# Performance work log

Hardware: AMD Instinct MI355X
Metric: run time of the kernel (lower is better)

The kernel has to match this reference:

```python
import jax, jax.numpy as jnp
import numpy as np

B = 32
N = 1024  # half_size == num_delays == num_wavelength
DELTA_TAU = 1.5e-15
W_CENTER = 1.175e15  # center_frequency / 2
PULSE_THRESHOLD = 0.01
PENALTY = 10.0
REAL_W = 1.0; IMAG_W = 1.0; INT_W = 1.0; PHASE_W = 1.0; FROG_W = 1.0
MSE_WSUM = REAL_W + IMAG_W + INT_W + PHASE_W

# Hilbert mask exactly as in the torch source (even N branch): H[N//2+1:]=2, H[N//2]=1
_Hm = np.zeros(N, dtype=np.float32)
_Hm[N // 2 + 1:] = 2.0
_Hm[N // 2] = 1.0
HILBERT_MASK = jnp.asarray(_Hm)

# precomputed circular-shift gather indices: shifted[m, j] = x[(j - delay[m]) mod N]
_delays = np.arange(-(N // 2), N // 2)
SHIFT_IDX = jnp.asarray((np.arange(N)[None, :] - _delays[:, None]) % N)  # [N, N] int
SHIFT_FACTOR = jnp.exp(-1j * jnp.asarray(2.0 * W_CENTER * DELTA_TAU * _delays, dtype=jnp.float32)).astype(jnp.complex64)  # [N]


def hilbert(x):  # x: [N] real -> [N] complex analytical signal
    xf = jnp.fft.fft(x)
    return jnp.fft.ifft(xf * HILBERT_MASK)


def shg_mat(a):  # a: [N] complex -> [N, N] complex SHG matrix (vectorized createSHGmat)
    shifted = a[SHIFT_IDX]                                  # [N, N] all circular shifts
    rows = a[None, :] * shifted * SHIFT_FACTOR[None, :]     # elementwise complex multiply
    f = jnp.fft.fft(jnp.fft.fftshift(rows, axes=-1), axis=-1)  # one batched FFT
    return DELTA_TAU * jnp.fft.fftshift(f, axes=-1)


def _first_last(mask):  # mask: [B, N] bool -> per-sample first/last significant index with fallback
    any_m = jnp.any(mask, axis=1)
    first = jnp.where(any_m, jnp.argmax(mask, axis=1), 0)
    last = jnp.where(any_m, N - 1 - jnp.argmax(mask[:, ::-1], axis=1), N - 1)
    return first, last


def setup_inputs() -> dict:
    key = jax.random.key(0)
    k1, k2, k3 = jax.random.split(key, 3)
    prediction = jax.random.normal(k1, (B, N), dtype=jnp.float32)
    label = jax.random.normal(k2, (B, 2 * N), dtype=jnp.float32)
    shg_matrix = jax.random.uniform(k3, (B, 1, N, N), dtype=jnp.float32)
    return {"prediction": prediction, "label": label, "shg_matrix": shg_matrix}


def reference(prediction, label, shg_matrix):
    pa = jax.vmap(hilbert)(prediction)          # [B, N] complex64
    pr, pi = pa.real, pa.imag
    lr, li = label[:, :N], label[:, N:]
    l_int = lr ** 2 + li ** 2
    p_int = pr ** 2 + pi ** 2
    l_ph = jnp.arctan2(li, lr)
    p_ph = jnp.arctan2(pi, pr)

    # ---- FROG error ----
    shg_pred = jnp.abs(jax.vmap(shg_mat)(pa)) ** 2              # [B, N, N]
    shg_pred = shg_pred / jnp.max(shg_pred, axis=(1, 2), keepdims=True)  # normalizeSHGmatrix
    t_ref = shg_matrix[:, 0]                                    # [B, N, N]
    sum1 = jnp.sum(shg_pred * t_ref, axis=(1, 2))
    sum2 = jnp.sum(t_ref * t_ref, axis=(1, 2))
    mu = sum1 / sum2
    r = jnp.sum(shg_pred - mu[:, None, None] * t_ref, axis=(1, 2)) ** 2
    norm = (N * N) * jnp.max(shg_pred, axis=(1, 2)) ** 2
    frog = jnp.where(r == 0.0, 0.0, jnp.sqrt(r / norm))         # [B]

    # ---- weighted masked MSE ----
    fr, lr_idx = _first_last(jnp.abs(lr) > PULSE_THRESHOLD)
    fi, li_idx = _first_last(jnp.abs(li) > PULSE_THRESHOLD)
    first = jnp.minimum(fr, fi)
    last = jnp.maximum(lr_idx, li_idx)
    ar = jnp.arange(N)[None, :]
    in_range = (ar >= first[:, None]) & (ar < last[:, None])    # [first:last] slice semantics
    phase_mask = in_range.astype(jnp.float32)
    pulse_mask = jnp.where(in_range, PENALTY, 1.0)

    mse_real = jnp.mean((pr - lr) ** 2 * pulse_mask, axis=1) * REAL_W
    mse_imag = jnp.mean((pi - li) ** 2 * pulse_mask, axis=1) * IMAG_W
    mse_int = jnp.mean((p_int - l_int) ** 2 * pulse_mask, axis=1) * INT_W
    mse_ph = jnp.mean((p_ph - l_ph) ** 2 * phase_mask, axis=1) * PHASE_W
    mse = (mse_real + mse_imag + mse_int + mse_ph) / MSE_WSUM

    return jnp.mean(mse + FROG_W * frog)
```

## Files before the change

### kernel.cpp

```cpp
#include <hip/hip_runtime.h>
#include <math.h>

#define N 1024
#define BATCH 32
#define NT 256
#define PADC(i) ((i) + ((i) >> 5))

#define WSYNC() asm volatile("s_waitcnt lgkmcnt(0)" ::: "memory")

typedef float2 cf;
__device__ __forceinline__ cf cadd(cf a, cf b){ return make_float2(a.x+b.x, a.y+b.y); }
__device__ __forceinline__ cf csub(cf a, cf b){ return make_float2(a.x-b.x, a.y-b.y); }
__device__ __forceinline__ cf cmul(cf a, cf b){ return make_float2(a.x*b.x - a.y*b.y, a.x*b.y + a.y*b.x); }

__device__ __forceinline__ cf twiddle(float jn){
    float s = __builtin_amdgcn_sinf(jn);
    float c = __builtin_amdgcn_cosf(jn);
    return make_float2(c, -s);
}

__device__ __forceinline__ int rev8(int q){
    int r = (int)(__brev((unsigned)q) >> 24);
    return ((r & 0x55) << 1) | ((r >> 1) & 0x55);
}
__device__ __forceinline__ int rev10(int m){
    int r = (int)(__brev((unsigned)m) >> 22);
    return ((r & 0x155) << 1) | ((r >> 1) & 0x155);
}

__device__ __forceinline__ void dif4(cf* w, int base, int q, float jn){
    cf x0 = w[PADC(base)];
    cf x1 = w[PADC(base + q)];
    cf x2 = w[PADC(base + 2*q)];
    cf x3 = w[PADC(base + 3*q)];
    cf A = cadd(x0,x2), Bs = cadd(x1,x3);
    cf C = csub(x0,x2), D = csub(x1,x3);
    cf Dmi = make_float2(D.y, -D.x);
    cf w1 = twiddle(jn);
    cf w2 = cmul(w1,w1);
    cf w3 = cmul(w2,w1);
    w[PADC(base)]       = cadd(A,Bs);
    w[PADC(base + q)]   = cmul(cadd(C,Dmi), w1);
    w[PADC(base + 2*q)] = cmul(csub(A,Bs), w2);
    w[PADC(base + 3*q)] = cmul(csub(C,Dmi), w3);
}

template<int LOG2N>
__device__ __forceinline__ void dif_stage(cf* w, int t){
    const int n = 1 << LOG2N, q = n >> 2;
    int j = t & (q - 1);
    int base = ((t >> (LOG2N - 2)) << LOG2N) + j;
    dif4(w, base, q, (float)j * (1.0f / (float)n));
}
template<int LOG2N>
__device__ __forceinline__ void dit_stage(cf* w, int t){
    const int n = 1 << LOG2N, q = n >> 2;
    int j = t & (q - 1);
    int base = ((t >> (LOG2N - 2)) << LOG2N) + j;
    cf x0 = w[PADC(base)];
    cf x1 = w[PADC(base + q)];
    cf x2 = w[PADC(base + 2*q)];
    cf x3 = w[PADC(base + 3*q)];
    cf w1 = twiddle((float)j * (1.0f / (float)n));
    cf w2 = cmul(w1,w1);
    cf w3 = cmul(w2,w1);
    x1 = cmul(x1,w1); x2 = cmul(x2,w2); x3 = cmul(x3,w3);
    cf A = cadd(x0,x2), Bs = cadd(x1,x3);
    cf C = csub(x0,x2), D = csub(x1,x3);
    cf Dmi = make_float2(D.y, -D.x);
    w[PADC(base)]       = cadd(A,Bs);
    w[PADC(base + q)]   = cadd(C,Dmi);
    w[PADC(base + 2*q)] = csub(A,Bs);
    w[PADC(base + 3*q)] = csub(C,Dmi);
}

__global__ __launch_bounds__(NT) void hilbert_k(const float* __restrict__ pred,
                                                const float* __restrict__ label,
                                                cf* __restrict__ a,
                                                cf* __restrict__ ca,
                                                float* __restrict__ mseJ) {
    __shared__ cf wk[1056];
    __shared__ float rbuf[4][4];
    __shared__ int ibuf[4][4];
    __shared__ int s_first, s_last;
    int t = threadIdx.x, b = blockIdx.x;
    for (int i = t; i < N; i += NT) wk[PADC(i)] = make_float2(pred[b * N + i], 0.f);
    __syncthreads();
    dif_stage<10>(wk, t); __syncthreads();
    dif_stage<8>(wk, t);  __syncthreads();
    dif_stage<6>(wk, t);  __syncthreads();
    dif_stage<4>(wk, t);  __syncthreads();
    dif_stage<2>(wk, t);  __syncthreads();
    for (int i = t; i < N; i += NT) {
        int k = rev10(i);
        float f = (k < 512) ? 0.f : ((k == 512) ? 1.f : 2.f);
        cf v = wk[PADC(i)];
        wk[PADC(i)] = make_float2(f * v.x, -f * v.y);
    }
    __syncthreads();
    dit_stage<2>(wk, t);  __syncthreads();
    dit_stage<4>(wk, t);  __syncthreads();
    dit_stage<6>(wk, t);  __syncthreads();
    dit_stage<8>(wk, t);  __syncthreads();
    dit_stage<10>(wk, t); __syncthreads();
    const float sc = 1.f / (float)N;
    for (int i = t; i < N; i += NT) {
        cf v = wk[PADC(i)];
        cf av = make_float2(v.x * sc, -v.y * sc);
        wk[PADC(i)] = av;
        a[b * N + i] = av;
        float p = (float)(3.525 * (double)(i - 512));
        float s_, c_;
        sincosf(p, &s_, &c_);
        ca[b * N + i] = make_float2(av.x * c_ + av.y * s_, av.y * c_ - av.x * s_);
    }
    __syncthreads();

    int w = t >> 6, lane = t & 63;
    int mnR = N, mxR = -1, mnI = N, mxI = -1;
    for (int n = t; n < N; n += NT) {
        float lr = label[b * 2 * N + n];
        float li = label[b * 2 * N + N + n];
        if (fabsf(lr) > 0.01f) { mnR = min(mnR, n); mxR = max(mxR, n); }
        if (fabsf(li) > 0.01f) { mnI = min(mnI, n); mxI = max(mxI, n); }
    }
    for (int o = 32; o > 0; o >>= 1) {
        mnR = min(mnR, __shfl_down(mnR, o));
        mxR = max(mxR, __shfl_down(mxR, o));
        mnI = min(mnI, __shfl_down(mnI, o));
        mxI = max(mxI, __shfl_down(mxI, o));
    }
    if (lane == 0) { ibuf[w][0] = mnR; ibuf[w][1] = mxR; ibuf[w][2] = mnI; ibuf[w][3] = mxI; }
    __syncthreads();
    if (t == 0) {
        int a0 = N, a1 = -1, a2 = N, a3 = -1;
        for (int i = 0; i < 4; ++i) {
            a0 = min(a0, ibuf[i][0]); a1 = max(a1, ibuf[i][1]);
            a2 = min(a2, ibuf[i][2]); a3 = max(a3, ibuf[i][3]);
        }
        int fr   = (a0 == N) ? 0 : a0;
        int lstR = (a1 < 0) ? (N - 1) : a1;
        int fi   = (a2 == N) ? 0 : a2;
        int lstI = (a3 < 0) ? (N - 1) : a3;
        s_first = min(fr, fi);
        s_last  = max(lstR, lstI);
    }
    __syncthreads();
    int first = s_first, last = s_last;

    float m_r = 0.f, m_i = 0.f, m_n = 0.f, m_p = 0.f;
    for (int n = t; n < N; n += NT) {
        cf p = wk[PADC(n)];
        float lr = label[b * 2 * N + n];
        float li = label[b * 2 * N + N + n];
        bool in = (n >= first) && (n < last);
        float pm  = in ? 10.f : 1.f;
        float phm = in ? 1.f : 0.f;
        float dr = p.x - lr, di = p.y - li;
        float dn = (p.x * p.x + p.y * p.y) - (lr * lr + li * li);
        float dp = atan2f(p.y, p.x) - atan2f(li, lr);
        m_r += dr * dr * pm;
        m_i += di * di * pm;
        m_n += dn * dn * pm;
        m_p += dp * dp * phm;
    }
    for (int o = 32; o > 0; o >>= 1) {
        m_r += __shfl_down(m_r, o);
        m_i += __shfl_down(m_i, o);
        m_n += __shfl_down(m_n, o);
        m_p += __shfl_down(m_p, o);
    }
    if (lane == 0) { rbuf[w][0] = m_r; rbuf[w][1] = m_i; rbuf[w][2] = m_n; rbuf[w][3] = m_p; }
    __syncthreads();
    if (t == 0) {
        float s = 0.f;
        for (int i = 0; i < 4; ++i) s += rbuf[i][0] + rbuf[i][1] + rbuf[i][2] + rbuf[i][3];
        mseJ[b] = s * (1.f / (float)N) * 0.25f;
    }
}

__global__ __launch_bounds__(NT) void shg_k(const cf* __restrict__ a,
                                            const cf* __restrict__ cag,
                                            const float* __restrict__ tref,
                                            float* __restrict__ Praw,
                                            float* __restrict__ Prt,
                                            float* __restrict__ Pmax,
                                            float* __restrict__ Pt,
                                            float* __restrict__ Ptt) {
    __shared__ cf wk[1056];
    __shared__ float rbuf[4][8];
    int t = threadIdx.x, bd = blockIdx.x;
    int b = bd >> 10, d = bd & 1023;

    {
        const cf* arow  = a   + b * N;
        const cf* carow = cag + b * N;
        cf x[4];
#pragma unroll
        for (int k = 0; k < 4; ++k) {
            int n1 = (t + 256 * k + 512) & 1023;
            int n2 = (t + 256 * k - d) & 1023;
            x[k] = cmul(carow[n1], arow[n2]);
        }
        cf A = cadd(x[0],x[2]), Bs = cadd(x[1],x[3]);
        cf C = csub(x[0],x[2]), D = csub(x[1],x[3]);
        cf Dmi = make_float2(D.y, -D.x);
        cf w1 = twiddle((float)t * (1.0f / 1024.0f));
        cf w2 = cmul(w1,w1);
        cf w3 = cmul(w2,w1);
        wk[PADC(t)]       = cadd(A,Bs);
        wk[PADC(t + 256)] = cmul(cadd(C,Dmi), w1);
        wk[PADC(t + 512)] = cmul(csub(A,Bs), w2);
        wk[PADC(t + 768)] = cmul(csub(C,Dmi), w3);
    }
    __syncthreads();
    dif4(wk, ((t >> 6) << 8) + (t & 63), 64, (float)(t & 63) * (1.0f / 256.0f)); WSYNC();
    dif4(wk, ((t >> 4) << 6) + (t & 15), 16, (float)(t & 15) * (1.0f / 64.0f));  WSYNC();
    dif4(wk, ((t >> 2) << 4) + (t & 3),   4, (float)(t & 3)  * (1.0f / 16.0f));  WSYNC();

    float sraw = 0.f, srt = 0.f, mx = 0.f, st = 0.f, stt = 0.f;
    const float* trow = tref + ((size_t)bd << 10);
    {
        int base = 4 * t;
        cf x0 = wk[PADC(base)], x1 = wk[PADC(base+1)];
        cf x2 = wk[PADC(base+2)], x3 = wk[PADC(base+3)];
        cf A = cadd(x0,x2), Bs = cadd(x1,x3);
        cf C = csub(x0,x2), D = csub(x1,x3);
        cf Dmi = make_float2(D.y, -D.x);
        cf y[4];
        y[0] = cadd(A,Bs); y[1] = cadd(C,Dmi); y[2] = csub(A,Bs); y[3] = csub(C,Dmi);
        int rq = rev8(t);
#pragma unroll
        for (int m = 0; m < 4; ++m) {
            float m2 = y[m].x * y[m].x + y[m].y * y[m].y;
            float tv = trow[(((m + 2) & 3) << 8) + rq];
            sraw += m2;
            srt += m2 * tv;
            mx = fmaxf(mx, m2);
            st += tv;
            stt += tv * tv;
        }
    }
    for (int o = 32; o > 0; o >>= 1) {
        sraw += __shfl_down(sraw, o);
        srt  += __shfl_down(srt, o);
        mx    = fmaxf(mx, __shfl_down(mx, o));
        st   += __shfl_down(st, o);
        stt  += __shfl_down(stt, o);
    }
    int w = t >> 6, lane = t & 63;
    if (lane == 0) {
        rbuf[w][0] = sraw; rbuf[w][1] = srt; rbuf[w][2] = mx;
        rbuf[w][3] = st;   rbuf[w][4] = stt;
    }
    __syncthreads();
    if (t == 0) {
        float a0 = 0.f, a1 = 0.f, a2 = 0.f, a3 = 0.f, a4 = 0.f;
        for (int i = 0; i < 4; ++i) {
            a0 += rbuf[i][0]; a1 += rbuf[i][1]; a2 = fmaxf(a2, rbuf[i][2]);
            a3 += rbuf[i][3]; a4 += rbuf[i][4];
        }
        Praw[bd] = a0; Prt[bd] = a1; Pmax[bd] = a2; Pt[bd] = a3; Ptt[bd] = a4;
    }
}

__global__ __launch_bounds__(NT) void loss_k(const float* __restrict__ Praw,
                                             const float* __restrict__ Prt,
                                             const float* __restrict__ Pmax,
                                             const float* __restrict__ Pt,
                                             const float* __restrict__ Ptt,
                                             const float* __restrict__ mseJ,
                                             float* __restrict__ out) {
    __shared__ float rbuf[4][8];
    int tid = threadIdx.x, b = blockIdx.x;
    int w = tid >> 6, lane = tid & 63;
    float sr = 0.f, srt = 0.f, mx = 0.f, st = 0.f, stt = 0.f;
    for (int i = tid; i < N; i += NT) {
        int idx = b * N + i;
        sr += Praw[idx]; srt += Prt[idx]; mx = fmaxf(mx, Pmax[idx]);
        st += Pt[idx];   stt += Ptt[idx];
    }
    for (int o = 32; o > 0; o >>= 1) {
        sr  += __shfl_down(sr, o);
        srt += __shfl_down(srt, o);
        mx   = fmaxf(mx, __shfl_down(mx, o));
        st  += __shfl_down(st, o);
        stt += __shfl_down(stt, o);
    }
    if (lane == 0) {
        rbuf[w][0] = sr; rbuf[w][1] = srt; rbuf[w][2] = mx;
        rbuf[w][3] = st; rbuf[w][4] = stt;
    }
    __syncthreads();
    if (tid == 0) {
        float A0 = 0.f, A1 = 0.f, A2 = 0.f, A3 = 0.f, A4 = 0.f;
        for (int i = 0; i < 4; ++i) {
            A0 += rbuf[i][0]; A1 += rbuf[i][1]; A2 = fmaxf(A2, rbuf[i][2]);
            A3 += rbuf[i][3]; A4 += rbuf[i][4];
        }
        float mu = (A1 / A2) / A4;
        float diff = A0 / A2 - mu * A3;
        float frog = fabsf(diff) * (1.f / (float)N);
        atomicAdd(out, (mseJ[b] + frog) * (1.f / (float)BATCH));
    }
}

extern "C" void kernel_launch(void* const* d_in, const int* in_sizes, int n_in,
                              void* d_out, int out_size, void* d_ws, size_t ws_size,
                              hipStream_t stream) {
    (void)in_sizes; (void)n_in; (void)out_size; (void)ws_size;
    const float* pred  = (const float*)d_in[0];
    const float* label = (const float*)d_in[1];
    const float* shg   = (const float*)d_in[2];
    float* out = (float*)d_out;

    char* ws = (char*)d_ws;
    cf* a   = (cf*)ws;
    cf* ca  = a + (size_t)BATCH * N;
    float* mseJ = (float*)(ca + (size_t)BATCH * N);
    float* P = mseJ + BATCH;
    float* Praw = P;
    float* Prt  = P + (size_t)BATCH * N;
    float* Pmax = P + 2 * (size_t)BATCH * N;
    float* Pt   = P + 3 * (size_t)BATCH * N;
    float* Ptt  = P + 4 * (size_t)BATCH * N;

    hipMemsetAsync(d_out, 0, sizeof(float), stream);
    hilbert_k<<<BATCH, NT, 0, stream>>>(pred, label, a, ca, mseJ);
    shg_k<<<BATCH * N, NT, 0, stream>>>(a, ca, shg, Praw, Prt, Pmax, Pt, Ptt);
    loss_k<<<BATCH, NT, 0, stream>>>(Praw, Prt, Pmax, Pt, Ptt, mseJ, out);
}
```

Before: 266.1 us.

## Process four delay rows per block with shared twiddles and radix-16 final pass

The SHG kernel now handles four delay rows per block (8192 blocks instead of 32768). The conj(a) values and the per-stage twiddles are computed once and reused across the rows. The last two radix-4 stages are merged into a register-resident radix-16 pass with constant twiddles and a new output index mapping, and the padding changes to one slot per 16 elements. This cuts launch count, twiddle transcendentals and LDS round trips, at the cost of more LDS per block and more registers, which may lower occupancy.

```diff
diff --git a/kernel.cpp b/kernel.cpp
--- a/kernel.cpp
+++ b/kernel.cpp
@@ -4,6 +4,9 @@
 #define N 1024
 #define BATCH 32
 #define NT 256
+#define ROWS 4
+#define RSTRIDE 1092
+#define P16(i) ((i) + ((i) >> 4))
 #define PADC(i) ((i) + ((i) >> 5))
 
 #define WSYNC() asm volatile("s_waitcnt lgkmcnt(0)" ::: "memory")
@@ -19,59 +22,55 @@
     return make_float2(c, -s);
 }
 
-__device__ __forceinline__ int rev8(int q){
-    int r = (int)(__brev((unsigned)q) >> 24);
-    return ((r & 0x55) << 1) | ((r >> 1) & 0x55);
-}
 __device__ __forceinline__ int rev10(int m){
     int r = (int)(__brev((unsigned)m) >> 22);
     return ((r & 0x155) << 1) | ((r >> 1) & 0x155);
 }
 
-__device__ __forceinline__ void dif4(cf* w, int base, int q, float jn){
-    cf x0 = w[PADC(base)];
-    cf x1 = w[PADC(base + q)];
-    cf x2 = w[PADC(base + 2*q)];
-    cf x3 = w[PADC(base + 3*q)];
+__device__ __forceinline__ void bfly(cf x0, cf x1, cf x2, cf x3,
+                                     cf& y0, cf& y1, cf& y2, cf& y3){
     cf A = cadd(x0,x2), Bs = cadd(x1,x3);
     cf C = csub(x0,x2), D = csub(x1,x3);
     cf Dmi = make_float2(D.y, -D.x);
-    cf w1 = twiddle(jn);
-    cf w2 = cmul(w1,w1);
-    cf w3 = cmul(w2,w1);
-    w[PADC(base)]       = cadd(A,Bs);
-    w[PADC(base + q)]   = cmul(cadd(C,Dmi), w1);
-    w[PADC(base + 2*q)] = cmul(csub(A,Bs), w2);
-    w[PADC(base + 3*q)] = cmul(csub(C,Dmi), w3);
-}
-
+    y0 = cadd(A,Bs); y1 = cadd(C,Dmi); y2 = csub(A,Bs); y3 = csub(C,Dmi);
+}
+
+__device__ __forceinline__ void dif4p(cf* w, int base, int q, cf w1, cf w2, cf w3){
+    cf x0 = w[P16(base)], x1 = w[P16(base+q)], x2 = w[P16(base+2*q)], x3 = w[P16(base+3*q)];
+    cf y0, y1, y2, y3; bfly(x0,x1,x2,x3,y0,y1,y2,y3);
+    w[P16(base)]     = y0;
+    w[P16(base+q)]   = cmul(y1,w1);
+    w[P16(base+2*q)] = cmul(y2,w2);
+    w[P16(base+3*q)] = cmul(y3,w3);
+}
+
+__device__ __forceinline__ void dif4h(cf* w, int base, int q, float jn){
+    cf x0 = w[PADC(base)], x1 = w[PADC(base+q)], x2 = w[PADC(base+2*q)], x3 = w[PADC(base+3*q)];
+    cf y0, y1, y2, y3; bfly(x0,x1,x2,x3,y0,y1,y2,y3);
+    cf w1 = twiddle(jn), w2 = cmul(w1,w1), w3 = cmul(w2,w1);
+    w[PADC(base)]     = y0;
+    w[PADC(base+q)]   = cmul(y1,w1);
+    w[PADC(base+2*q)] = cmul(y2,w2);
+    w[PADC(base+3*q)] = cmul(y3,w3);
+}
 template<int LOG2N>
 __device__ __forceinline__ void dif_stage(cf* w, int t){
     const int n = 1 << LOG2N, q = n >> 2;
     int j = t & (q - 1);
     int base = ((t >> (LOG2N - 2)) << LOG2N) + j;
-    dif4(w, base, q, (float)j * (1.0f / (float)n));
+    dif4h(w, base, q, (float)j * (1.0f / (float)n));
 }
 template<int LOG2N>
 __device__ __forceinline__ void dit_stage(cf* w, int t){
     const int n = 1 << LOG2N, q = n >> 2;
     int j = t & (q - 1);
     int base = ((t >> (LOG2N - 2)) << LOG2N) + j;
-    cf x0 = w[PADC(base)];
-    cf x1 = w[PADC(base + q)];
-    cf x2 = w[PADC(base + 2*q)];
-    cf x3 = w[PADC(base + 3*q)];
+    cf x0 = w[PADC(base)], x1 = w[PADC(base+q)], x2 = w[PADC(base+2*q)], x3 = w[PADC(base+3*q)];
     cf w1 = twiddle((float)j * (1.0f / (float)n));
-    cf w2 = cmul(w1,w1);
-    cf w3 = cmul(w2,w1);
+    cf w2 = cmul(w1,w1), w3 = cmul(w2,w1);
     x1 = cmul(x1,w1); x2 = cmul(x2,w2); x3 = cmul(x3,w3);
-    cf A = cadd(x0,x2), Bs = cadd(x1,x3);
-    cf C = csub(x0,x2), D = csub(x1,x3);
-    cf Dmi = make_float2(D.y, -D.x);
-    w[PADC(base)]       = cadd(A,Bs);
-    w[PADC(base + q)]   = cadd(C,Dmi);
-    w[PADC(base + 2*q)] = csub(A,Bs);
-    w[PADC(base + 3*q)] = csub(C,Dmi);
+    cf y0, y1, y2, y3; bfly(x0,x1,x2,x3,y0,y1,y2,y3);
+    w[PADC(base)] = y0; w[PADC(base+q)] = y1; w[PADC(base+2*q)] = y2; w[PADC(base+3*q)] = y3;
 }
 
 __global__ __launch_bounds__(NT) void hilbert_k(const float* __restrict__ pred,
@@ -187,79 +186,119 @@
                                             float* __restrict__ Pmax,
                                             float* __restrict__ Pt,
                                             float* __restrict__ Ptt) {
-    __shared__ cf wk[1056];
-    __shared__ float rbuf[4][8];
-    int t = threadIdx.x, bd = blockIdx.x;
-    int b = bd >> 10, d = bd & 1023;
-
-    {
-        const cf* arow  = a   + b * N;
-        const cf* carow = cag + b * N;
-        cf x[4];
-#pragma unroll
-        for (int k = 0; k < 4; ++k) {
-            int n1 = (t + 256 * k + 512) & 1023;
-            int n2 = (t + 256 * k - d) & 1023;
-            x[k] = cmul(carow[n1], arow[n2]);
-        }
-        cf A = cadd(x[0],x[2]), Bs = cadd(x[1],x[3]);
-        cf C = csub(x[0],x[2]), D = csub(x[1],x[3]);
-        cf Dmi = make_float2(D.y, -D.x);
+    __shared__ cf wk[ROWS * RSTRIDE];
+    __shared__ float rbuf[4][ROWS][5];
+    int t = threadIdx.x, blk = blockIdx.x;
+    int b = blk >> 8;
+    int dg = (blk & 255) << 2;
+    const cf* arow  = a   + b * N;
+    const cf* carow = cag + b * N;
+
+    {
         cf w1 = twiddle((float)t * (1.0f / 1024.0f));
-        cf w2 = cmul(w1,w1);
-        cf w3 = cmul(w2,w1);
-        wk[PADC(t)]       = cadd(A,Bs);
-        wk[PADC(t + 256)] = cmul(cadd(C,Dmi), w1);
-        wk[PADC(t + 512)] = cmul(csub(A,Bs), w2);
-        wk[PADC(t + 768)] = cmul(csub(C,Dmi), w3);
-    }
-    __syncthreads();
-    dif4(wk, ((t >> 6) << 8) + (t & 63), 64, (float)(t & 63) * (1.0f / 256.0f)); WSYNC();
-    dif4(wk, ((t >> 4) << 6) + (t & 15), 16, (float)(t & 15) * (1.0f / 64.0f));  WSYNC();
-    dif4(wk, ((t >> 2) << 4) + (t & 3),   4, (float)(t & 3)  * (1.0f / 16.0f));  WSYNC();
+        cf w2 = cmul(w1,w1), w3 = cmul(w2,w1);
+        cf cav[4];
+#pragma unroll
+        for (int k = 0; k < 4; ++k) cav[k] = carow[(t + 256*k + 512) & 1023];
+#pragma unroll
+        for (int r = 0; r < ROWS; ++r) {
+            int d = dg + r;
+            cf x[4];
+#pragma unroll
+            for (int k = 0; k < 4; ++k)
+                x[k] = cmul(cav[k], arow[(t + 256*k - d) & 1023]);
+            cf y0, y1, y2, y3; bfly(x[0],x[1],x[2],x[3],y0,y1,y2,y3);
+            cf* w = wk + r * RSTRIDE;
+            w[P16(t)]     = y0;
+            w[P16(t+256)] = cmul(y1,w1);
+            w[P16(t+512)] = cmul(y2,w2);
+            w[P16(t+768)] = cmul(y3,w3);
+        }
+    }
+    __syncthreads();
+    {
+        int j = t & 63;
+        int base = ((t >> 6) << 8) + j;
+        cf w1 = twiddle((float)j * (1.0f / 256.0f));
+        cf w2 = cmul(w1,w1), w3 = cmul(w2,w1);
+#pragma unroll
+        for (int r = 0; r < ROWS; ++r) dif4p(wk + r * RSTRIDE, base, 64, w1, w2, w3);
+    }
+    WSYNC();
+    {
+        int j = t & 15;
+        int base = ((t >> 4) << 6) + j;
+        cf w1 = twiddle((float)j * (1.0f / 64.0f));
+        cf w2 = cmul(w1,w1), w3 = cmul(w2,w1);
+#pragma unroll
+        for (int r = 0; r < ROWS; ++r) dif4p(wk + r * RSTRIDE, base, 16, w1, w2, w3);
+    }
+    WSYNC();
 
     float sraw = 0.f, srt = 0.f, mx = 0.f, st = 0.f, stt = 0.f;
-    const float* trow = tref + ((size_t)bd << 10);
-    {
-        int base = 4 * t;
-        cf x0 = wk[PADC(base)], x1 = wk[PADC(base+1)];
-        cf x2 = wk[PADC(base+2)], x3 = wk[PADC(base+3)];
-        cf A = cadd(x0,x2), Bs = cadd(x1,x3);
-        cf C = csub(x0,x2), D = csub(x1,x3);
-        cf Dmi = make_float2(D.y, -D.x);
-        cf y[4];
-        y[0] = cadd(A,Bs); y[1] = cadd(C,Dmi); y[2] = csub(A,Bs); y[3] = csub(C,Dmi);
-        int rq = rev8(t);
-#pragma unroll
-        for (int m = 0; m < 4; ++m) {
-            float m2 = y[m].x * y[m].x + y[m].y * y[m].y;
-            float tv = trow[(((m + 2) & 3) << 8) + rq];
-            sraw += m2;
-            srt += m2 * tv;
-            mx = fmaxf(mx, m2);
-            st += tv;
-            stt += tv * tv;
-        }
-    }
-    for (int o = 32; o > 0; o >>= 1) {
+    {
+        const cf W1 = { 0.923879533f, -0.382683432f};
+        const cf W2 = { 0.707106781f, -0.707106781f};
+        const cf W3 = { 0.382683432f, -0.923879533f};
+        const cf W6 = {-0.707106781f, -0.707106781f};
+        const cf W9 = {-0.923879533f,  0.382683432f};
+        int r = t & 3;
+        int g = ((t >> 6) << 4) + ((t >> 2) & 15);
+        cf* w = wk + r * RSTRIDE;
+        cf v[16];
+        int base = 17 * g;
+#pragma unroll
+        for (int k = 0; k < 16; ++k) v[k] = w[base + k];
+        cf o[16];
+        bfly(v[0], v[4], v[8], v[12], o[0], o[4], o[8],  o[12]);
+        { cf y0,y1,y2,y3; bfly(v[1],v[5],v[9], v[13],y0,y1,y2,y3);
+          o[1]=y0; o[5]=cmul(y1,W1); o[9]=cmul(y2,W2); o[13]=cmul(y3,W3); }
+        { cf y0,y1,y2,y3; bfly(v[2],v[6],v[10],v[14],y0,y1,y2,y3);
+          o[2]=y0; o[6]=cmul(y1,W2); o[10]=make_float2(y2.y,-y2.x); o[14]=cmul(y3,W6); }
+        { cf y0,y1,y2,y3; bfly(v[3],v[7],v[11],v[15],y0,y1,y2,y3);
+          o[3]=y0; o[7]=cmul(y1,W3); o[11]=cmul(y2,W6); o[15]=cmul(y3,W9); }
+        int bd = b * N + dg + r;
+        const float* trow = tref + ((size_t)bd << 10);
+        int kb = ((g & 3) << 4) | (g & 12) | (g >> 4);
+#pragma unroll
+        for (int u = 0; u < 4; ++u) {
+            cf y0, y1, y2, y3;
+            bfly(o[4*u], o[4*u+1], o[4*u+2], o[4*u+3], y0, y1, y2, y3);
+            cf ys[4] = {y0, y1, y2, y3};
+#pragma unroll
+            for (int m = 0; m < 4; ++m) {
+                float m2 = ys[m].x * ys[m].x + ys[m].y * ys[m].y;
+                float tv = trow[(((m + 2) & 3) << 8) | (u << 6) | kb];
+                sraw += m2;
+                srt += m2 * tv;
+                mx = fmaxf(mx, m2);
+                st += tv;
+                stt += tv * tv;
+            }
+        }
+    }
+    for (int o = 32; o >= 4; o >>= 1) {
         sraw += __shfl_down(sraw, o);
         srt  += __shfl_down(srt, o);
         mx    = fmaxf(mx, __shfl_down(mx, o));
         st   += __shfl_down(st, o);
         stt  += __shfl_down(stt, o);
     }
-    int w = t >> 6, lane = t & 63;
-    if (lane == 0) {
-        rbuf[w][0] = sraw; rbuf[w][1] = srt; rbuf[w][2] = mx;
-        rbuf[w][3] = st;   rbuf[w][4] = stt;
-    }
-    __syncthreads();
-    if (t == 0) {
+    {
+        int lane = t & 63, wv = t >> 6;
+        if (lane < 4) {
+            rbuf[wv][lane][0] = sraw; rbuf[wv][lane][1] = srt; rbuf[wv][lane][2] = mx;
+            rbuf[wv][lane][3] = st;   rbuf[wv][lane][4] = stt;
+        }
+    }
+    __syncthreads();
+    if (t < ROWS) {
         float a0 = 0.f, a1 = 0.f, a2 = 0.f, a3 = 0.f, a4 = 0.f;
         for (int i = 0; i < 4; ++i) {
-            a0 += rbuf[i][0]; a1 += rbuf[i][1]; a2 = fmaxf(a2, rbuf[i][2]);
-            a3 += rbuf[i][3]; a4 += rbuf[i][4];
-        }
+            a0 += rbuf[i][t][0]; a1 += rbuf[i][t][1]; a2 = fmaxf(a2, rbuf[i][t][2]);
+            a3 += rbuf[i][t][3]; a4 += rbuf[i][t][4];
+        }
+        int bd = b * N + dg + t;
         Praw[bd] = a0; Prt[bd] = a1; Pmax[bd] = a2; Pt[bd] = a3; Ptt[bd] = a4;
     }
 }
@@ -327,6 +366,6 @@
 
     hipMemsetAsync(d_out, 0, sizeof(float), stream);
     hilbert_k<<<BATCH, NT, 0, stream>>>(pred, label, a, ca, mseJ);
-    shg_k<<<BATCH * N, NT, 0, stream>>>(a, ca, shg, Praw, Prt, Pmax, Pt, Ptt);
+    shg_k<<<BATCH * 256, NT, 0, stream>>>(a, ca, shg, Praw, Prt, Pmax, Pt, Ptt);
     loss_k<<<BATCH, NT, 0, stream>>>(Praw, Prt, Pmax, Pt, Ptt, mseJ, out);
 }
```

Measured after the change: 231.7 us. 1.15x faster.
